# Performance work log

Hardware: AMD Instinct MI355X
Metric: run time of the kernel (lower is better)

## Reference

```python
import jax, jax.numpy as jnp
import numpy as np

THR = 0.5
IOU_THR = 0.2
K = 4096          # fixed pre-NMS candidate budget (jit-compatible stand-in for thr filtering + full sort)
FEAT_OFF = 5      # cols: 0 obj score, 1:5 box (l,t,r,b), 5: class-feature embedding


def setup_inputs() -> dict:
    key = jax.random.key(0)
    kx, kl, kt, kw, kh, ks, kp, kr = jax.random.split(key, 8)
    C, H, W = 261, 320, 320  # 5 + 256 feature channels
    x = jax.random.normal(kx, (1, C, H, W), dtype=jnp.float32)
    # plausible (l,t,r,b) boxes in padded-image coordinates so NMS has real work
    l = jax.random.uniform(kl, (1, 1, H, W), dtype=jnp.float32) * 600.0
    t = jax.random.uniform(kt, (1, 1, H, W), dtype=jnp.float32) * 600.0
    r = l + jax.random.uniform(kw, (1, 1, H, W), dtype=jnp.float32) * 60.0
    b = t + jax.random.uniform(kh, (1, 1, H, W), dtype=jnp.float32) * 60.0
    x = x.at[:, 1:5].set(jnp.concatenate([l, t, r, b], axis=1))
    state_matrix = jax.random.normal(ks, (16, 256), dtype=jnp.float32)
    padding = jax.random.uniform(kp, (2,), dtype=jnp.float32) * 10.0
    ratio = jax.random.uniform(kr, (1,), dtype=jnp.float32) * 0.6 + 0.4
    return {"x": x, "state_matrix": state_matrix, "padding": padding,
            "ratio": ratio, "image_width": 1280, "image_height": 768}


def _pairwise_iou(boxes, eps=1e-10):
    # boxes: [K, 4] as (l, t, r, b); returns [K, K]
    l, t, r, b = boxes[:, 0], boxes[:, 1], boxes[:, 2], boxes[:, 3]
    area = (r - l) * (b - t)
    iw = jnp.clip(jnp.minimum(r[:, None], r[None, :]) - jnp.maximum(l[:, None], l[None, :]), 0.0)
    ih = jnp.clip(jnp.minimum(b[:, None], b[None, :]) - jnp.maximum(t[:, None], t[None, :]), 0.0)
    inter = iw * ih
    union = area[:, None] + area[None, :] - inter + eps
    return inter / union


def reference(x, state_matrix, padding, ratio, image_width, image_height):
    B, C, H, W = x.shape
    out = x[0].reshape(C, H * W).T                      # [N, C]
    sig = jax.nn.sigmoid(out[:, 0])                     # sigmoid on objectness channel
    cls_logits = out[:, FEAT_OFF:] @ state_matrix.T     # [N, 16] class-state matmul
    cls_val = jnp.max(cls_logits, axis=1)
    cls_idx = jnp.argmax(cls_logits, axis=1)
    score = sig * cls_val                               # out[:,0] * cls_values
    valid = sig > THR                                   # out[0] > thr filter
    score = jnp.where(valid, score, -jnp.inf)
    topv, topi = jax.lax.top_k(score, K)                # descending sort, fixed budget
    boxes = out[topi, 1:5]                              # [K, 4] (l,t,r,b)
    cls_k = cls_idx[topi]
    area = (boxes[:, 2] - boxes[:, 0]) * (boxes[:, 3] - boxes[:, 1])
    iou = _pairwise_iou(boxes)                          # [K, K]

    alive0 = jnp.isfinite(topv)                         # only thr-passing candidates enter the queue
    kept0 = jnp.zeros((K,), dtype=bool)

    def body(carry, i):
        alive, kept = carry
        is_cur = alive[i]                               # still in the queue (not suppressed earlier)
        alive = alive.at[i].set(False)                  # pop top
        ious_i = iou[i]
        n_over = jnp.sum((ious_i >= IOU_THR) & alive)   # remaining boxes with iou >= thr
        accept = is_cur & (area[i] >= 4.0) & (n_over >= 10)
        kept = kept.at[i].set(accept)
        alive = jnp.where(accept, alive & (ious_i < IOU_THR), alive)  # suppress only on accept
        return (alive, kept), None

    (_, kept), _ = jax.lax.scan(body, (alive0, kept0), jnp.arange(K))

    keep = kept & (topv >= THR)                         # p[0,0] < thr -> skip
    inv_r = 1.0 / ratio[0]
    x1 = jnp.maximum((boxes[:, 0] - padding[0]) * inv_r, 0.0)
    y1 = jnp.maximum((boxes[:, 1] - padding[1]) * inv_r, 0.0)
    x2 = jnp.minimum((boxes[:, 2] - padding[0]) * inv_r, jnp.float32(image_width))
    y2 = jnp.minimum((boxes[:, 3] - padding[1]) * inv_r, jnp.float32(image_height))
    keep = keep & (x1 < image_width) & (y1 < image_height)

    dets = jnp.stack([jnp.ones((K,), jnp.float32), topv, x1, y1, x2, y2,
                      cls_k.astype(jnp.float32)], axis=1)   # [K, 7]
    dets = jnp.where(keep[:, None], dets, 0.0)
    return dets
```

## Files before the change

kernel.cpp:

```cpp
#include <hip/hip_runtime.h>
#include <hip/hip_bf16.h>
#include <math.h>

#define HW 102400
#define KSEL 4096
#define CAP 16384

__device__ inline unsigned fkey(float f) {
    unsigned u = __float_as_uint(f);
    return (u & 0x80000000u) ? ~u : (u | 0x80000000u);
}

__device__ inline unsigned wave_sum64_s(unsigned x) {
    x += (unsigned)__builtin_amdgcn_update_dpp(0, (int)x, 0x111, 0xf, 0xf, false);
    x += (unsigned)__builtin_amdgcn_update_dpp(0, (int)x, 0x112, 0xf, 0xf, false);
    x += (unsigned)__builtin_amdgcn_update_dpp(0, (int)x, 0x114, 0xf, 0xf, false);
    x += (unsigned)__builtin_amdgcn_update_dpp(0, (int)x, 0x118, 0xf, 0xf, false);
    x += (unsigned)__builtin_amdgcn_update_dpp(0, (int)x, 0x142, 0xa, 0xf, false);
    x += (unsigned)__builtin_amdgcn_update_dpp(0, (int)x, 0x143, 0xc, 0xf, false);
    return (unsigned)__builtin_amdgcn_readlane((int)x, 63);
}

__device__ inline unsigned long long readlane64(unsigned long long v, int l) {
    unsigned lo = (unsigned)__builtin_amdgcn_readlane((int)(unsigned)(v & 0xffffffffull), l);
    unsigned hi = (unsigned)__builtin_amdgcn_readlane((int)(unsigned)(v >> 32), l);
    return ((unsigned long long)hi << 32) | lo;
}

__global__ __launch_bounds__(256) void k_score(const float* __restrict__ x,
                                               const float* __restrict__ sm,
                                               float* __restrict__ score,
                                               int* __restrict__ clsidx) {
    __shared__ float swt[256][16];
    __shared__ float tile[2][16][256];
    int t = threadIdx.x;
    for (int i = t; i < 4096; i += 256) {
        int k = i >> 8, c = i & 255;
        swt[c][k] = sm[i];
    }
    int wave = t >> 6, lane = t & 63;
    size_t pxb = (size_t)blockIdx.x * 256;
    const float* xc = x + (size_t)5 * HW + pxb;

    float acc[16];
#pragma unroll
    for (int k = 0; k < 16; ++k) acc[k] = 0.f;

    float4 sa[4], sb[4];

#define LOADX(dst, ti)                                                         \
    _Pragma("unroll") for (int j = 0; j < 4; ++j)                              \
        dst[j] = *(const float4*)(xc + (size_t)((ti) * 16 + wave * 4 + j) * HW + lane * 4);
#define STOREX(src, s)                                                         \
    _Pragma("unroll") for (int j = 0; j < 4; ++j)                              \
        ((float4*)&tile[s][wave * 4 + j][0])[lane] = src[j];
#define COMP(s, ti)                                                            \
    _Pragma("unroll") for (int cc = 0; cc < 16; ++cc) {                        \
        float xv = tile[s][cc][t];                                             \
        const float4* w4 = (const float4*)&swt[(ti) * 16 + cc][0];             \
        float4 w0 = w4[0], w1 = w4[1], w2 = w4[2], w3 = w4[3];                 \
        acc[0]  = fmaf(xv, w0.x, acc[0]);  acc[1]  = fmaf(xv, w0.y, acc[1]);   \
        acc[2]  = fmaf(xv, w0.z, acc[2]);  acc[3]  = fmaf(xv, w0.w, acc[3]);   \
        acc[4]  = fmaf(xv, w1.x, acc[4]);  acc[5]  = fmaf(xv, w1.y, acc[5]);   \
        acc[6]  = fmaf(xv, w1.z, acc[6]);  acc[7]  = fmaf(xv, w1.w, acc[7]);   \
        acc[8]  = fmaf(xv, w2.x, acc[8]);  acc[9]  = fmaf(xv, w2.y, acc[9]);   \
        acc[10] = fmaf(xv, w2.z, acc[10]); acc[11] = fmaf(xv, w2.w, acc[11]);  \
        acc[12] = fmaf(xv, w3.x, acc[12]); acc[13] = fmaf(xv, w3.y, acc[13]);  \
        acc[14] = fmaf(xv, w3.z, acc[14]); acc[15] = fmaf(xv, w3.w, acc[15]);  \
    }

    LOADX(sa, 0);
    STOREX(sa, 0);
    LOADX(sa, 1);
    LOADX(sb, 2);
    __syncthreads();

#pragma unroll
    for (int k = 0; k < 16; k += 2) {
        COMP(k & 1, k);
        STOREX(sa, (k + 1) & 1);
        if (k + 3 < 16) LOADX(sa, k + 3);
        __syncthreads();
        COMP((k + 1) & 1, k + 1);
        if (k + 2 < 16) { STOREX(sb, k & 1); }
        if (k + 4 < 16) LOADX(sb, k + 4);
        __syncthreads();
    }
#undef LOADX
#undef STOREX
#undef COMP

    float mv = acc[0]; int mi = 0;
#pragma unroll
    for (int k = 1; k < 16; ++k)
        if (acc[k] > mv) { mv = acc[k]; mi = k; }
    int n = (int)pxb + t;
    float x0 = x[n];
    float sig = 1.0f / (1.0f + expf(-x0));
    float sc = (sig > 0.5f) ? sig * mv : -INFINITY;
    score[n] = sc;
    clsidx[n] = mi;
}

__global__ void k_hist(const float* __restrict__ score, unsigned* __restrict__ hist) {
    int n = blockIdx.x * 256 + threadIdx.x;
    float sc = score[n];
    if (sc != -INFINITY) atomicAdd(&hist[fkey(sc) >> 16], 1u);
}

__global__ __launch_bounds__(1024) void k_findp(const unsigned* __restrict__ hist,
                                                unsigned* __restrict__ meta) {
    __shared__ unsigned part[1024];
    __shared__ unsigned sgrp, s_after;
    __shared__ unsigned bins[64];
    int t = threadIdx.x;
    if (t == 0) { sgrp = 0; s_after = 0; }
    unsigned s = 0;
    const unsigned* hp = hist + t * 64;
    for (int i = 0; i < 64; ++i) s += hp[i];
    part[t] = s;
    __syncthreads();
    for (int off = 1; off < 1024; off <<= 1) {
        unsigned v = (t + off < 1024) ? part[t + off] : 0u;
        __syncthreads();
        part[t] += v;
        __syncthreads();
    }
    if (part[t] >= KSEL && (t == 1023 || part[t + 1] < KSEL)) {
        sgrp = (unsigned)t;
        s_after = (t == 1023) ? 0u : part[t + 1];
    }
    __syncthreads();
    unsigned g = sgrp, SA = s_after;
    if (t < 64) bins[t] = hist[g * 64 + t];
    __syncthreads();
    if (t == 0) {
        unsigned acc = SA, p = g * 64;
        for (int b = 63; b >= 0; --b) {
            acc += bins[b];
            if (acc >= KSEL) { p = g * 64 + (unsigned)b; break; }
        }
        meta[1] = p;
    }
}

__global__ void k_collect(const float* __restrict__ score,
                          unsigned* __restrict__ meta,
                          unsigned long long* __restrict__ cand) {
    int n = blockIdx.x * 256 + threadIdx.x;
    unsigned key = fkey(score[n]);
    if ((key >> 16) >= meta[1]) {
        unsigned pos = atomicAdd(&meta[0], 1u);
        if (pos < CAP)
            cand[pos] = ((unsigned long long)key << 32) | (unsigned)(~(unsigned)n);
    }
}

__global__ __launch_bounds__(256) void k_rank(const unsigned long long* __restrict__ cand,
                                              const unsigned* __restrict__ meta,
                                              const float* __restrict__ x,
                                              const float* __restrict__ score,
                                              const int* __restrict__ clsidx,
                                              float* __restrict__ topv,
                                              float* __restrict__ bl, float* __restrict__ bt,
                                              float* __restrict__ br, float* __restrict__ bb,
                                              float* __restrict__ area, int* __restrict__ clsk) {
    __shared__ unsigned long long tile[1024];
    int C = (int)meta[0]; if (C > CAP) C = CAP;
    int j = blockIdx.x * 256 + threadIdx.x;
    unsigned long long kj = (j < C) ? cand[j] : 0ull;
    unsigned rank = 0;
    for (int tb = 0; tb < C; tb += 1024) {
        int cnt = min(1024, C - tb);
        __syncthreads();
        for (int u = threadIdx.x; u < cnt; u += 256) tile[u] = cand[tb + u];
        __syncthreads();
        if (j < C)
            for (int u = 0; u < cnt; ++u) rank += (tile[u] > kj) ? 1u : 0u;
    }
    if (j < C && rank < KSEL) {
        unsigned n = ~(unsigned)(kj & 0xFFFFFFFFull);
        float l  = x[(size_t)1 * HW + n];
        float tt = x[(size_t)2 * HW + n];
        float r  = x[(size_t)3 * HW + n];
        float b  = x[(size_t)4 * HW + n];
        topv[rank] = score[n];
        bl[rank] = l; bt[rank] = tt; br[rank] = r; bb[rank] = b;
        area[rank] = (r - l) * (b - tt);
        clsk[rank] = clsidx[n];
    }
}

__global__ __launch_bounds__(256) void k_mask(const float* __restrict__ bl, const float* __restrict__ bt,
                                              const float* __restrict__ br, const float* __restrict__ bb,
                                              const float* __restrict__ area,
                                              unsigned long long* __restrict__ mask) {
    __shared__ float sl[256], st[256], sr[256], sb[256], sa[256];
    int t = threadIdx.x;
    int ic = blockIdx.x >> 4;
    int jc = blockIdx.x & 15;
    int i = ic * 256 + t;
    int j0 = jc * 256;
    sl[t] = bl[j0 + t]; st[t] = bt[j0 + t]; sr[t] = br[j0 + t];
    sb[t] = bb[j0 + t]; sa[t] = area[j0 + t];
    __syncthreads();
    float li = bl[i], ti = bt[i], ri = br[i], bi = bb[i], ai = area[i];
#pragma unroll
    for (int w = 0; w < 4; ++w) {
        unsigned long long m = 0;
        for (int k2 = 0; k2 < 64; ++k2) {
            int j = w * 64 + k2;
            float iw = fminf(ri, sr[j]) - fmaxf(li, sl[j]); iw = fmaxf(iw, 0.f);
            float ih = fminf(bi, sb[j]) - fmaxf(ti, st[j]); ih = fmaxf(ih, 0.f);
            float inter = iw * ih;
            float uni = ai + sa[j] - inter + 1e-10f;
            if (inter / uni >= 0.2f) m |= (1ull << k2);
        }
        mask[(size_t)i * 64 + (jc * 4 + w)] = m;
    }
}

__global__ __launch_bounds__(256, 1) void k_nms(const unsigned long long* __restrict__ mask,
                                                const float* __restrict__ topv,
                                                const float* __restrict__ area,
                                                unsigned long long* __restrict__ keptW) {
    __shared__ unsigned long long rowsL[2][4096];
    __shared__ unsigned long long aliveL[64];
    __shared__ unsigned cntL[64];
    int t = threadIdx.x;
    int lane = t & 63;
    int W = t >> 6;
    int g = t & 3;
    int jrow = t >> 2;

    unsigned long long alive = 0, areaok = 0, keptAcc = 0;
    if (W == 0) {
        for (int k = 0; k < 64; ++k) {
            float tv = topv[(size_t)k * 64 + lane];
            float ar = area[(size_t)k * 64 + lane];
            unsigned long long b1 = __ballot(tv != -INFINITY);
            unsigned long long b2 = __ballot(ar >= 4.0f);
            if (lane == k) { alive = b1; areaok = b2; }
        }
        aliveL[lane] = alive;
    }

#define STAGE(bb, s)                                                            \
    do {                                                                        \
        _Pragma("unroll") for (int i = 0; i < 8; ++i) {                         \
            int seg_ = i * 4 + W;                                               \
            int r_ = seg_ * 2 + (lane >> 5);                                    \
            int p_ = (lane & 31) * 2;                                           \
            int wl_ = (p_ - 2 * r_) & 63;                                       \
            const unsigned long long* gp_ =                                     \
                mask + ((size_t)((bb) * 64 + r_) * 64 + wl_);                   \
            __builtin_amdgcn_global_load_lds(                                   \
                (const __attribute__((address_space(1))) void*)gp_,             \
                (__attribute__((address_space(3))) void*)&rowsL[s][seg_ * 128], \
                16, 0, 0);                                                      \
        }                                                                       \
    } while (0)

    STAGE(0, 0);
    STAGE(1, 1);

#define VER(jj, rw)                                                             \
    {                                                                           \
        unsigned long long awc = readlane64(alive, b);                          \
        if ((awc >> (jj)) & 1ull) {                                             \
            unsigned long long awAdj = alive;                                   \
            unsigned long long pm = ((jj) == 63) ? ~0ull                        \
                                                 : ((1ull << ((jj) + 1)) - 1ull); \
            if (lane == b) awAdj &= ~pm;                                        \
            unsigned c_ = (unsigned)__popcll((rw) & awAdj);                     \
            unsigned tt_ = wave_sum64_s(c_);                                    \
            if (tt_ >= 10u) { alive &= ~(rw); keptB |= 1ull << (jj); }          \
        }                                                                       \
    }

    for (int b = 0; b < 64; ++b) {
        if (b < 63) asm volatile("s_waitcnt vmcnt(8)" ::: "memory");
        else        asm volatile("s_waitcnt vmcnt(0)" ::: "memory");
        __builtin_amdgcn_sched_barrier(0);
        __builtin_amdgcn_s_barrier();

        const unsigned long long* rb = &rowsL[b & 1][0];

        unsigned long long pfxj = (jrow == 63) ? ~0ull : ((1ull << (jrow + 1)) - 1ull);
        int base_w = g * 16;
        unsigned cnt = 0;
#pragma unroll
        for (int q = 0; q < 8; ++q) {
            int wl = base_w + q * 2;
            int ph = (wl + 2 * jrow) & 63;
            ulonglong2 rv = *(const ulonglong2*)&rb[jrow * 64 + ph];
            ulonglong2 av = *(const ulonglong2*)&aliveL[wl];
            unsigned cx = (unsigned)__popcll(rv.x & av.x);
            unsigned cy = (unsigned)__popcll(rv.y & av.y);
            cnt += cx + cy;
            if (wl == b)     cnt -= (unsigned)__popcll(rv.x & av.x & pfxj);
            if (wl + 1 == b) cnt -= (unsigned)__popcll(rv.y & av.y & pfxj);
        }
        cnt += (unsigned)__builtin_amdgcn_update_dpp(0, (int)cnt, 0xB1, 0xf, 0xf, false);
        cnt += (unsigned)__builtin_amdgcn_update_dpp(0, (int)cnt, 0x4E, 0xf, 0xf, false);
        if (g == 0) cntL[jrow] = cnt;
        asm volatile("s_waitcnt lgkmcnt(0)" ::: "memory");
        __builtin_amdgcn_s_barrier();

        if (W == 0) {
            unsigned long long keptB = 0;
            unsigned long long aw0snap = readlane64(alive, b);
            unsigned long long areaok0 = readlane64(areaok, b);
            unsigned myc = cntL[lane];
            bool candp = (myc >= 10u) && ((areaok0 >> lane) & 1ull) &&
                         ((aw0snap >> lane) & 1ull);
            unsigned long long cand = __ballot(candp);
            while (cand) {
                int j1 = __ffsll(cand) - 1; cand &= cand - 1;
                int j2 = -1, j3 = -1, j4 = -1;
                if (cand) { j2 = __ffsll(cand) - 1; cand &= cand - 1; }
                if (cand) { j3 = __ffsll(cand) - 1; cand &= cand - 1; }
                if (cand) { j4 = __ffsll(cand) - 1; cand &= cand - 1; }
                unsigned long long r1 = rb[j1 * 64 + ((lane + 2 * j1) & 63)];
                unsigned long long r2 = (j2 >= 0) ? rb[j2 * 64 + ((lane + 2 * j2) & 63)] : 0;
                unsigned long long r3 = (j3 >= 0) ? rb[j3 * 64 + ((lane + 2 * j3) & 63)] : 0;
                unsigned long long r4 = (j4 >= 0) ? rb[j4 * 64 + ((lane + 2 * j4) & 63)] : 0;
                VER(j1, r1);
                if (j2 >= 0) VER(j2, r2);
                if (j3 >= 0) VER(j3, r3);
                if (j4 >= 0) VER(j4, r4);
            }
            if (lane == b) { alive = 0; keptAcc = keptB; }
            aliveL[lane] = alive;
        }
        asm volatile("s_waitcnt lgkmcnt(0)" ::: "memory");
        __builtin_amdgcn_s_barrier();
        if (b + 2 < 64) STAGE(b + 2, b & 1);
    }
    if (W == 0) keptW[lane] = keptAcc;
#undef STAGE
#undef VER
}

__global__ __launch_bounds__(256) void k_out(const unsigned long long* __restrict__ keptW,
                                             const float* __restrict__ topv,
                                             const float* __restrict__ bl, const float* __restrict__ bt,
                                             const float* __restrict__ br, const float* __restrict__ bb,
                                             const int* __restrict__ clsk,
                                             const float* __restrict__ padding,
                                             const float* __restrict__ ratio,
                                             const int* __restrict__ piw, const int* __restrict__ pih,
                                             float* __restrict__ out) {
    int i = blockIdx.x * 256 + threadIdx.x;
    if (i >= KSEL) return;
    bool kept = (keptW[i >> 6] >> (i & 63)) & 1ull;
    float tv = topv[i];
    bool keep = kept && (tv >= 0.5f);
    float p0 = padding[0], p1 = padding[1];
    float invr = 1.0f / ratio[0];
    float W_ = (float)piw[0], H_ = (float)pih[0];
    float x1 = fmaxf((bl[i] - p0) * invr, 0.f);
    float y1 = fmaxf((bt[i] - p1) * invr, 0.f);
    float x2 = fminf((br[i] - p0) * invr, W_);
    float y2 = fminf((bb[i] - p1) * invr, H_);
    keep = keep && (x1 < W_) && (y1 < H_);
    float* o = out + (size_t)i * 7;
    if (keep) {
        o[0] = 1.0f; o[1] = tv; o[2] = x1; o[3] = y1; o[4] = x2; o[5] = y2;
        o[6] = (float)clsk[i];
    } else {
        o[0] = 0.f; o[1] = 0.f; o[2] = 0.f; o[3] = 0.f; o[4] = 0.f; o[5] = 0.f; o[6] = 0.f;
    }
}

extern "C" void kernel_launch(void* const* d_in, const int* in_sizes, int n_in,
                              void* d_out, int out_size, void* d_ws, size_t ws_size,
                              hipStream_t stream) {
    const float* x       = (const float*)d_in[0];
    const float* sm      = (const float*)d_in[1];
    const float* padding = (const float*)d_in[2];
    const float* ratio   = (const float*)d_in[3];
    const int*   piw     = (const int*)d_in[4];
    const int*   pih     = (const int*)d_in[5];
    float* out = (float*)d_out;
    char* ws = (char*)d_ws;

    float* score               = (float*)(ws + 0);
    int*   clsidx              = (int*)(ws + 409600);
    unsigned* hist             = (unsigned*)(ws + 819200);
    unsigned* meta             = (unsigned*)(ws + 1081344);
    unsigned long long* cand   = (unsigned long long*)(ws + 1081856);
    float* topv                = (float*)(ws + 1212928);
    float* bl                  = (float*)(ws + 1229312);
    float* bt                  = (float*)(ws + 1245696);
    float* br                  = (float*)(ws + 1262080);
    float* bb                  = (float*)(ws + 1278464);
    float* area                = (float*)(ws + 1294848);
    int*   clsk                = (int*)(ws + 1311232);
    unsigned long long* keptW  = (unsigned long long*)(ws + 1327616);
    unsigned long long* mask   = (unsigned long long*)(ws + 1328128);

    hipMemsetAsync(hist, 0, 262144 + 512, stream);

    k_score  <<<400, 256, 0, stream>>>(x, sm, score, clsidx);
    k_hist   <<<400, 256, 0, stream>>>(score, hist);
    k_findp  <<<1, 1024, 0, stream>>>(hist, meta);
    k_collect<<<400, 256, 0, stream>>>(score, meta, cand);
    k_rank   <<<CAP / 256, 256, 0, stream>>>(cand, meta, x, score, clsidx,
                                             topv, bl, bt, br, bb, area, clsk);
    k_mask   <<<256, 256, 0, stream>>>(bl, bt, br, bb, area, mask);
    k_nms    <<<1, 256, 0, stream>>>(mask, topv, area, keptW);
    k_out    <<<16, 256, 0, stream>>>(keptW, topv, bl, bt, br, bb, clsk,
                                      padding, ratio, piw, pih, out);
}
```

Baseline: 324.7 us.

## Overlap NMS prescan with serial verification, fuse histogram and output kernels

The histogram atomic moves into the scoring kernel, and the output-writing kernel is folded into the tail of the NMS kernel, removing two launches. The NMS loop is restructured so wave 0 runs the serial verification for block b while waves 1-3 precompute alive-overlap counts for block b+1. A third LDS stage buffer deepens the mask prefetch. The added cost is that the prescan for block b+1 reads alive bits from before block b's suppression; the code appears to rely on the exact VER recheck for correctness. The output loop also now runs on a single block.

```diff
diff --git a/kernel.cpp b/kernel.cpp
--- a/kernel.cpp
+++ b/kernel.cpp
@@ -30,7 +30,8 @@
 __global__ __launch_bounds__(256) void k_score(const float* __restrict__ x,
                                                const float* __restrict__ sm,
                                                float* __restrict__ score,
-                                               int* __restrict__ clsidx) {
+                                               int* __restrict__ clsidx,
+                                               unsigned* __restrict__ hist) {
     __shared__ float swt[256][16];
     __shared__ float tile[2][16][256];
     int t = threadIdx.x;
@@ -100,11 +101,6 @@
     float sc = (sig > 0.5f) ? sig * mv : -INFINITY;
     score[n] = sc;
     clsidx[n] = mi;
-}
-
-__global__ void k_hist(const float* __restrict__ score, unsigned* __restrict__ hist) {
-    int n = blockIdx.x * 256 + threadIdx.x;
-    float sc = score[n];
     if (sc != -INFINITY) atomicAdd(&hist[fkey(sc) >> 16], 1u);
 }
 
@@ -223,32 +219,25 @@
 __global__ __launch_bounds__(256, 1) void k_nms(const unsigned long long* __restrict__ mask,
                                                 const float* __restrict__ topv,
                                                 const float* __restrict__ area,
-                                                unsigned long long* __restrict__ keptW) {
-    __shared__ unsigned long long rowsL[2][4096];
+                                                const float* __restrict__ bl, const float* __restrict__ bt,
+                                                const float* __restrict__ br, const float* __restrict__ bb,
+                                                const int* __restrict__ clsk,
+                                                const float* __restrict__ padding,
+                                                const float* __restrict__ ratio,
+                                                const int* __restrict__ piw, const int* __restrict__ pih,
+                                                float* __restrict__ out) {
+    __shared__ unsigned long long rowsL[3][4096];
     __shared__ unsigned long long aliveL[64];
-    __shared__ unsigned cntL[64];
+    __shared__ unsigned long long keptL[64];
+    __shared__ unsigned cntP[2][64][3];
     int t = threadIdx.x;
     int lane = t & 63;
     int W = t >> 6;
-    int g = t & 3;
-    int jrow = t >> 2;
-
-    unsigned long long alive = 0, areaok = 0, keptAcc = 0;
-    if (W == 0) {
-        for (int k = 0; k < 64; ++k) {
-            float tv = topv[(size_t)k * 64 + lane];
-            float ar = area[(size_t)k * 64 + lane];
-            unsigned long long b1 = __ballot(tv != -INFINITY);
-            unsigned long long b2 = __ballot(ar >= 4.0f);
-            if (lane == k) { alive = b1; areaok = b2; }
-        }
-        aliveL[lane] = alive;
-    }
 
 #define STAGE(bb, s)                                                            \
     do {                                                                        \
-        _Pragma("unroll") for (int i = 0; i < 8; ++i) {                         \
-            int seg_ = i * 4 + W;                                               \
+        _Pragma("unroll") for (int i_ = 0; i_ < 8; ++i_) {                      \
+            int seg_ = i_ * 4 + W;                                              \
             int r_ = seg_ * 2 + (lane >> 5);                                    \
             int p_ = (lane & 31) * 2;                                           \
             int wl_ = (p_ - 2 * r_) & 63;                                       \
@@ -261,60 +250,81 @@
         }                                                                       \
     } while (0)
 
+#define PRESCAN(BB)                                                             \
+    do {                                                                        \
+        int u_ = t - 64;                                                        \
+        int j_ = u_ & 63;                                                       \
+        int p_ = u_ >> 6;                                                       \
+        const unsigned long long* rb_ = &rowsL[(BB) % 3][0];                    \
+        int q0_ = (p_ == 0) ? 0 : (p_ == 1) ? 11 : 22;                          \
+        int qN_ = (p_ == 2) ? 10 : 11;                                          \
+        unsigned long long pfx_ = (j_ == 63) ? ~0ull : ((1ull << (j_ + 1)) - 1ull); \
+        unsigned cnt_ = 0;                                                      \
+        for (int q_ = q0_; q_ < q0_ + qN_; ++q_) {                              \
+            int wl_ = q_ * 2;                                                   \
+            int ph_ = (wl_ + 2 * j_) & 63;                                      \
+            ulonglong2 rv_ = *(const ulonglong2*)&rb_[j_ * 64 + ph_];           \
+            ulonglong2 av_ = *(const ulonglong2*)&aliveL[wl_];                  \
+            unsigned long long ax_ = rv_.x & av_.x, ay_ = rv_.y & av_.y;        \
+            cnt_ += (unsigned)__popcll(ax_) + (unsigned)__popcll(ay_);          \
+            if (wl_ == (BB))     cnt_ -= (unsigned)__popcll(ax_ & pfx_);        \
+            if (wl_ + 1 == (BB)) cnt_ -= (unsigned)__popcll(ay_ & pfx_);        \
+        }                                                                       \
+        cntP[(BB) & 1][j_][p_] = cnt_;                                          \
+    } while (0)
+
+#define VER(jj, rw)                                                            \
+    {                                                                          \
+        unsigned long long awc = readlane64(alive, b);                         \
+        if ((awc >> (jj)) & 1ull) {                                            \
+            unsigned long long awAdj = alive;                                  \
+            unsigned long long pm = ((jj) == 63) ? ~0ull                       \
+                                                 : ((1ull << ((jj) + 1)) - 1ull); \
+            if (lane == b) awAdj &= ~pm;                                       \
+            unsigned c_ = (unsigned)__popcll((rw) & awAdj);                    \
+            unsigned tt_ = wave_sum64_s(c_);                                   \
+            if (tt_ >= 10u) { alive &= ~(rw); keptB |= 1ull << (jj); }         \
+        }                                                                      \
+    }
+
+    unsigned long long alive = 0, areaok = 0;
+    if (W == 0) {
+        for (int k = 0; k < 64; ++k) {
+            float tv = topv[(size_t)k * 64 + lane];
+            float ar = area[(size_t)k * 64 + lane];
+            unsigned long long b1 = __ballot(tv != -INFINITY);
+            unsigned long long b2 = __ballot(ar >= 4.0f);
+            if (lane == k) { alive = b1; areaok = b2; }
+        }
+    }
     STAGE(0, 0);
     STAGE(1, 1);
-
-#define VER(jj, rw)                                                             \
-    {                                                                           \
-        unsigned long long awc = readlane64(alive, b);                          \
-        if ((awc >> (jj)) & 1ull) {                                             \
-            unsigned long long awAdj = alive;                                   \
-            unsigned long long pm = ((jj) == 63) ? ~0ull                        \
-                                                 : ((1ull << ((jj) + 1)) - 1ull); \
-            if (lane == b) awAdj &= ~pm;                                        \
-            unsigned c_ = (unsigned)__popcll((rw) & awAdj);                     \
-            unsigned tt_ = wave_sum64_s(c_);                                    \
-            if (tt_ >= 10u) { alive &= ~(rw); keptB |= 1ull << (jj); }          \
-        }                                                                       \
-    }
+    if (W == 0) aliveL[lane] = alive;
+    asm volatile("s_waitcnt lgkmcnt(0)" ::: "memory");
+    asm volatile("s_waitcnt vmcnt(8)" ::: "memory");
+    __builtin_amdgcn_sched_barrier(0);
+    __builtin_amdgcn_s_barrier();
+
+    STAGE(2, 2);
+    if (W > 0) PRESCAN(0);
+    asm volatile("s_waitcnt lgkmcnt(0)" ::: "memory");
+    __builtin_amdgcn_s_barrier();
 
     for (int b = 0; b < 64; ++b) {
-        if (b < 63) asm volatile("s_waitcnt vmcnt(8)" ::: "memory");
-        else        asm volatile("s_waitcnt vmcnt(0)" ::: "memory");
+        if (b <= 61) asm volatile("s_waitcnt vmcnt(8)" ::: "memory");
+        else         asm volatile("s_waitcnt vmcnt(0)" ::: "memory");
         __builtin_amdgcn_sched_barrier(0);
         __builtin_amdgcn_s_barrier();
 
-        const unsigned long long* rb = &rowsL[b & 1][0];
-
-        unsigned long long pfxj = (jrow == 63) ? ~0ull : ((1ull << (jrow + 1)) - 1ull);
-        int base_w = g * 16;
-        unsigned cnt = 0;
-#pragma unroll
-        for (int q = 0; q < 8; ++q) {
-            int wl = base_w + q * 2;
-            int ph = (wl + 2 * jrow) & 63;
-            ulonglong2 rv = *(const ulonglong2*)&rb[jrow * 64 + ph];
-            ulonglong2 av = *(const ulonglong2*)&aliveL[wl];
-            unsigned cx = (unsigned)__popcll(rv.x & av.x);
-            unsigned cy = (unsigned)__popcll(rv.y & av.y);
-            cnt += cx + cy;
-            if (wl == b)     cnt -= (unsigned)__popcll(rv.x & av.x & pfxj);
-            if (wl + 1 == b) cnt -= (unsigned)__popcll(rv.y & av.y & pfxj);
-        }
-        cnt += (unsigned)__builtin_amdgcn_update_dpp(0, (int)cnt, 0xB1, 0xf, 0xf, false);
-        cnt += (unsigned)__builtin_amdgcn_update_dpp(0, (int)cnt, 0x4E, 0xf, 0xf, false);
-        if (g == 0) cntL[jrow] = cnt;
-        asm volatile("s_waitcnt lgkmcnt(0)" ::: "memory");
-        __builtin_amdgcn_s_barrier();
-
         if (W == 0) {
-            unsigned long long keptB = 0;
+            const unsigned long long* rb = &rowsL[b % 3][0];
+            unsigned myc = cntP[b & 1][lane][0] + cntP[b & 1][lane][1] + cntP[b & 1][lane][2];
             unsigned long long aw0snap = readlane64(alive, b);
             unsigned long long areaok0 = readlane64(areaok, b);
-            unsigned myc = cntL[lane];
             bool candp = (myc >= 10u) && ((areaok0 >> lane) & 1ull) &&
                          ((aw0snap >> lane) & 1ull);
             unsigned long long cand = __ballot(candp);
+            unsigned long long keptB = 0;
             while (cand) {
                 int j1 = __ffsll(cand) - 1; cand &= cand - 1;
                 int j2 = -1, j3 = -1, j4 = -1;
@@ -330,47 +340,40 @@
                 if (j3 >= 0) VER(j3, r3);
                 if (j4 >= 0) VER(j4, r4);
             }
-            if (lane == b) { alive = 0; keptAcc = keptB; }
+            if (lane == b) alive = 0;
+            if (lane == 0) keptL[b] = keptB;
             aliveL[lane] = alive;
+        } else if (b < 63) {
+            PRESCAN(b + 1);
         }
         asm volatile("s_waitcnt lgkmcnt(0)" ::: "memory");
         __builtin_amdgcn_s_barrier();
-        if (b + 2 < 64) STAGE(b + 2, b & 1);
-    }
-    if (W == 0) keptW[lane] = keptAcc;
-#undef STAGE
-#undef VER
-}
-
-__global__ __launch_bounds__(256) void k_out(const unsigned long long* __restrict__ keptW,
-                                             const float* __restrict__ topv,
-                                             const float* __restrict__ bl, const float* __restrict__ bt,
-                                             const float* __restrict__ br, const float* __restrict__ bb,
-                                             const int* __restrict__ clsk,
-                                             const float* __restrict__ padding,
-                                             const float* __restrict__ ratio,
-                                             const int* __restrict__ piw, const int* __restrict__ pih,
-                                             float* __restrict__ out) {
-    int i = blockIdx.x * 256 + threadIdx.x;
-    if (i >= KSEL) return;
-    bool kept = (keptW[i >> 6] >> (i & 63)) & 1ull;
-    float tv = topv[i];
-    bool keep = kept && (tv >= 0.5f);
+        if (b + 3 < 64) STAGE(b + 3, (b + 3) % 3);
+    }
+
     float p0 = padding[0], p1 = padding[1];
     float invr = 1.0f / ratio[0];
-    float W_ = (float)piw[0], H_ = (float)pih[0];
-    float x1 = fmaxf((bl[i] - p0) * invr, 0.f);
-    float y1 = fmaxf((bt[i] - p1) * invr, 0.f);
-    float x2 = fminf((br[i] - p0) * invr, W_);
-    float y2 = fminf((bb[i] - p1) * invr, H_);
-    keep = keep && (x1 < W_) && (y1 < H_);
-    float* o = out + (size_t)i * 7;
-    if (keep) {
-        o[0] = 1.0f; o[1] = tv; o[2] = x1; o[3] = y1; o[4] = x2; o[5] = y2;
-        o[6] = (float)clsk[i];
-    } else {
-        o[0] = 0.f; o[1] = 0.f; o[2] = 0.f; o[3] = 0.f; o[4] = 0.f; o[5] = 0.f; o[6] = 0.f;
-    }
+    float Wimg = (float)piw[0], Himg = (float)pih[0];
+    for (int i = t; i < KSEL; i += 256) {
+        bool kept = (keptL[i >> 6] >> (i & 63)) & 1ull;
+        float tv = topv[i];
+        bool keep = kept && (tv >= 0.5f);
+        float x1 = fmaxf((bl[i] - p0) * invr, 0.f);
+        float y1 = fmaxf((bt[i] - p1) * invr, 0.f);
+        float x2 = fminf((br[i] - p0) * invr, Wimg);
+        float y2 = fminf((bb[i] - p1) * invr, Himg);
+        keep = keep && (x1 < Wimg) && (y1 < Himg);
+        float* o = out + (size_t)i * 7;
+        if (keep) {
+            o[0] = 1.0f; o[1] = tv; o[2] = x1; o[3] = y1; o[4] = x2; o[5] = y2;
+            o[6] = (float)clsk[i];
+        } else {
+            o[0] = 0.f; o[1] = 0.f; o[2] = 0.f; o[3] = 0.f; o[4] = 0.f; o[5] = 0.f; o[6] = 0.f;
+        }
+    }
+#undef STAGE
+#undef PRESCAN
+#undef VER
 }
 
 extern "C" void kernel_launch(void* const* d_in, const int* in_sizes, int n_in,
@@ -397,19 +400,16 @@
     float* bb                  = (float*)(ws + 1278464);
     float* area                = (float*)(ws + 1294848);
     int*   clsk                = (int*)(ws + 1311232);
-    unsigned long long* keptW  = (unsigned long long*)(ws + 1327616);
     unsigned long long* mask   = (unsigned long long*)(ws + 1328128);
 
     hipMemsetAsync(hist, 0, 262144 + 512, stream);
 
-    k_score  <<<400, 256, 0, stream>>>(x, sm, score, clsidx);
-    k_hist   <<<400, 256, 0, stream>>>(score, hist);
+    k_score  <<<400, 256, 0, stream>>>(x, sm, score, clsidx, hist);
     k_findp  <<<1, 1024, 0, stream>>>(hist, meta);
     k_collect<<<400, 256, 0, stream>>>(score, meta, cand);
     k_rank   <<<CAP / 256, 256, 0, stream>>>(cand, meta, x, score, clsidx,
                                              topv, bl, bt, br, bb, area, clsk);
     k_mask   <<<256, 256, 0, stream>>>(bl, bt, br, bb, area, mask);
-    k_nms    <<<1, 256, 0, stream>>>(mask, topv, area, keptW);
-    k_out    <<<16, 256, 0, stream>>>(keptW, topv, bl, bt, br, bb, clsk,
-                                      padding, ratio, piw, pih, out);
-}
+    k_nms    <<<1, 256, 0, stream>>>(mask, topv, area, bl, bt, br, bb, clsk,
+                                     padding, ratio, piw, pih, out);
+}
```

Result: slower. 332.1 us (+2.3%).

## Fuse histogram into score kernel, fold output into NMS, use smaller score blocks

Applied to the files above, without the earlier changes.

The score kernel now builds the histogram with atomics itself, so the separate k_hist launch and its reread of the score array go away. The output-writing kernel is merged into the single-block NMS kernel, which keeps the kept bitmask in shared memory and writes detections directly. The score kernel moves to 128-thread blocks (800 blocks) with a different channel-to-thread load mapping, trading more blocks for finer spreading across CUs. Two launches are removed, but the output stage now runs on only one block.

```diff
diff --git a/kernel.cpp b/kernel.cpp
--- a/kernel.cpp
+++ b/kernel.cpp
@@ -27,19 +27,21 @@
     return ((unsigned long long)hi << 32) | lo;
 }
 
-__global__ __launch_bounds__(256) void k_score(const float* __restrict__ x,
+__global__ __launch_bounds__(128) void k_score(const float* __restrict__ x,
                                                const float* __restrict__ sm,
                                                float* __restrict__ score,
-                                               int* __restrict__ clsidx) {
+                                               int* __restrict__ clsidx,
+                                               unsigned* __restrict__ hist) {
     __shared__ float swt[256][16];
-    __shared__ float tile[2][16][256];
+    __shared__ float tile[2][16][128];
     int t = threadIdx.x;
-    for (int i = t; i < 4096; i += 256) {
+    for (int i = t; i < 4096; i += 128) {
         int k = i >> 8, c = i & 255;
         swt[c][k] = sm[i];
     }
-    int wave = t >> 6, lane = t & 63;
-    size_t pxb = (size_t)blockIdx.x * 256;
+    int cg = t >> 5;
+    int le = t & 31;
+    size_t pxb = (size_t)blockIdx.x * 128;
     const float* xc = x + (size_t)5 * HW + pxb;
 
     float acc[16];
@@ -50,10 +52,10 @@
 
 #define LOADX(dst, ti)                                                         \
     _Pragma("unroll") for (int j = 0; j < 4; ++j)                              \
-        dst[j] = *(const float4*)(xc + (size_t)((ti) * 16 + wave * 4 + j) * HW + lane * 4);
+        dst[j] = *(const float4*)(xc + (size_t)((ti) * 16 + 4 * j + cg) * HW + le * 4);
 #define STOREX(src, s)                                                         \
     _Pragma("unroll") for (int j = 0; j < 4; ++j)                              \
-        ((float4*)&tile[s][wave * 4 + j][0])[lane] = src[j];
+        ((float4*)&tile[s][4 * j + cg][0])[le] = src[j];
 #define COMP(s, ti)                                                            \
     _Pragma("unroll") for (int cc = 0; cc < 16; ++cc) {                        \
         float xv = tile[s][cc][t];                                             \
@@ -100,11 +102,6 @@
     float sc = (sig > 0.5f) ? sig * mv : -INFINITY;
     score[n] = sc;
     clsidx[n] = mi;
-}
-
-__global__ void k_hist(const float* __restrict__ score, unsigned* __restrict__ hist) {
-    int n = blockIdx.x * 256 + threadIdx.x;
-    float sc = score[n];
     if (sc != -INFINITY) atomicAdd(&hist[fkey(sc) >> 16], 1u);
 }
 
@@ -223,9 +220,16 @@
 __global__ __launch_bounds__(256, 1) void k_nms(const unsigned long long* __restrict__ mask,
                                                 const float* __restrict__ topv,
                                                 const float* __restrict__ area,
-                                                unsigned long long* __restrict__ keptW) {
+                                                const float* __restrict__ bl, const float* __restrict__ bt,
+                                                const float* __restrict__ br, const float* __restrict__ bb,
+                                                const int* __restrict__ clsk,
+                                                const float* __restrict__ padding,
+                                                const float* __restrict__ ratio,
+                                                const int* __restrict__ piw, const int* __restrict__ pih,
+                                                float* __restrict__ out) {
     __shared__ unsigned long long rowsL[2][4096];
     __shared__ unsigned long long aliveL[64];
+    __shared__ unsigned long long keptL[64];
     __shared__ unsigned cntL[64];
     int t = threadIdx.x;
     int lane = t & 63;
@@ -337,40 +341,31 @@
         __builtin_amdgcn_s_barrier();
         if (b + 2 < 64) STAGE(b + 2, b & 1);
     }
-    if (W == 0) keptW[lane] = keptAcc;
+    if (W == 0) keptL[lane] = keptAcc;
+    __syncthreads();
+
+    float p0 = padding[0], p1 = padding[1];
+    float invr = 1.0f / ratio[0];
+    float Wimg = (float)piw[0], Himg = (float)pih[0];
+    for (int i = t; i < KSEL; i += 256) {
+        bool kept = (keptL[i >> 6] >> (i & 63)) & 1ull;
+        float tv = topv[i];
+        bool keep = kept && (tv >= 0.5f);
+        float x1 = fmaxf((bl[i] - p0) * invr, 0.f);
+        float y1 = fmaxf((bt[i] - p1) * invr, 0.f);
+        float x2 = fminf((br[i] - p0) * invr, Wimg);
+        float y2 = fminf((bb[i] - p1) * invr, Himg);
+        keep = keep && (x1 < Wimg) && (y1 < Himg);
+        float* o = out + (size_t)i * 7;
+        if (keep) {
+            o[0] = 1.0f; o[1] = tv; o[2] = x1; o[3] = y1; o[4] = x2; o[5] = y2;
+            o[6] = (float)clsk[i];
+        } else {
+            o[0] = 0.f; o[1] = 0.f; o[2] = 0.f; o[3] = 0.f; o[4] = 0.f; o[5] = 0.f; o[6] = 0.f;
+        }
+    }
 #undef STAGE
 #undef VER
-}
-
-__global__ __launch_bounds__(256) void k_out(const unsigned long long* __restrict__ keptW,
-                                             const float* __restrict__ topv,
-                                             const float* __restrict__ bl, const float* __restrict__ bt,
-                                             const float* __restrict__ br, const float* __restrict__ bb,
-                                             const int* __restrict__ clsk,
-                                             const float* __restrict__ padding,
-                                             const float* __restrict__ ratio,
-                                             const int* __restrict__ piw, const int* __restrict__ pih,
-                                             float* __restrict__ out) {
-    int i = blockIdx.x * 256 + threadIdx.x;
-    if (i >= KSEL) return;
-    bool kept = (keptW[i >> 6] >> (i & 63)) & 1ull;
-    float tv = topv[i];
-    bool keep = kept && (tv >= 0.5f);
-    float p0 = padding[0], p1 = padding[1];
-    float invr = 1.0f / ratio[0];
-    float W_ = (float)piw[0], H_ = (float)pih[0];
-    float x1 = fmaxf((bl[i] - p0) * invr, 0.f);
-    float y1 = fmaxf((bt[i] - p1) * invr, 0.f);
-    float x2 = fminf((br[i] - p0) * invr, W_);
-    float y2 = fminf((bb[i] - p1) * invr, H_);
-    keep = keep && (x1 < W_) && (y1 < H_);
-    float* o = out + (size_t)i * 7;
-    if (keep) {
-        o[0] = 1.0f; o[1] = tv; o[2] = x1; o[3] = y1; o[4] = x2; o[5] = y2;
-        o[6] = (float)clsk[i];
-    } else {
-        o[0] = 0.f; o[1] = 0.f; o[2] = 0.f; o[3] = 0.f; o[4] = 0.f; o[5] = 0.f; o[6] = 0.f;
-    }
 }
 
 extern "C" void kernel_launch(void* const* d_in, const int* in_sizes, int n_in,
@@ -397,19 +392,16 @@
     float* bb                  = (float*)(ws + 1278464);
     float* area                = (float*)(ws + 1294848);
     int*   clsk                = (int*)(ws + 1311232);
-    unsigned long long* keptW  = (unsigned long long*)(ws + 1327616);
     unsigned long long* mask   = (unsigned long long*)(ws + 1328128);
 
     hipMemsetAsync(hist, 0, 262144 + 512, stream);
 
-    k_score  <<<400, 256, 0, stream>>>(x, sm, score, clsidx);
-    k_hist   <<<400, 256, 0, stream>>>(score, hist);
+    k_score  <<<800, 128, 0, stream>>>(x, sm, score, clsidx, hist);
     k_findp  <<<1, 1024, 0, stream>>>(hist, meta);
     k_collect<<<400, 256, 0, stream>>>(score, meta, cand);
     k_rank   <<<CAP / 256, 256, 0, stream>>>(cand, meta, x, score, clsidx,
                                              topv, bl, bt, br, bb, area, clsk);
     k_mask   <<<256, 256, 0, stream>>>(bl, bt, br, bb, area, mask);
-    k_nms    <<<1, 256, 0, stream>>>(mask, topv, area, keptW);
-    k_out    <<<16, 256, 0, stream>>>(keptW, topv, bl, bt, br, bb, clsk,
-                                      padding, ratio, piw, pih, out);
-}
+    k_nms    <<<1, 256, 0, stream>>>(mask, topv, area, bl, bt, br, bb, clsk,
+                                     padding, ratio, piw, pih, out);
+}
```

After: 312.2 us. 1.04x faster.
